# Kernel optimization log

Hardware: AMD Instinct MI355X
Metric: run time of the kernel (lower is better)

Reference implementation:

```python
import jax, jax.numpy as jnp
import numpy as np

LN_EPS = 1e-5

def _proj(x, w, b):
    # 1x1 conv: x [B,C,H,W], w [O,C], b [O]
    return jnp.einsum('bchw,oc->bohw', x, w) + b[None, :, None, None]

def _layernorm(x, w, b):
    # normalize over last dim
    mu = jnp.mean(x, axis=-1, keepdims=True)
    var = jnp.mean(jnp.square(x - mu), axis=-1, keepdims=True)
    return (x - mu) * jax.lax.rsqrt(var + LN_EPS) * w + b

def setup_inputs() -> dict:
    key = jax.random.key(0)
    ks = jax.random.split(key, 12)
    C = 256
    d = {
        's3': jax.random.normal(ks[0], (2, C, 64, 64), jnp.float32),
        's4': jax.random.normal(ks[1], (2, C, 32, 64), jnp.float32),
        's5': jax.random.normal(ks[2], (2, C, 16, 64), jnp.float32),
        'qw': jax.random.normal(ks[3], (C, C), jnp.float32) * 0.02,
        'qb': jax.random.normal(ks[4], (C,), jnp.float32) * 0.02,
        'kw': jax.random.normal(ks[5], (C, C), jnp.float32) * 0.02,
        'kb': jax.random.normal(ks[6], (C,), jnp.float32) * 0.02,
        'vw': jax.random.normal(ks[7], (C, C), jnp.float32) * 0.02,
        'vb': jax.random.normal(ks[8], (C,), jnp.float32) * 0.02,
        'ow': jax.random.normal(ks[9], (C, C), jnp.float32) * 0.02,
        'ob': jax.random.normal(ks[10], (C,), jnp.float32) * 0.02,
        'ln_w': jnp.ones((C,), jnp.float32),
        'ln_b': jnp.zeros((C,), jnp.float32),
    }
    return d

def reference(s3, s4, s5, qw, qb, kw, kb, vw, vb, ow, ob, ln_w, ln_b):
    B, C, H, W = s3.shape
    num_heads = 8
    head_dim = C // num_heads
    scale = head_dim ** -0.5

    q = _proj(s3, qw, qb).reshape(B, C, H * W)            # [B,C,Nq]
    k4 = _proj(s4, kw, kb).reshape(B, C, -1)
    k5 = _proj(s5, kw, kb).reshape(B, C, -1)
    v4 = _proj(s4, vw, vb).reshape(B, C, -1)
    v5 = _proj(s5, vw, vb).reshape(B, C, -1)
    k = jnp.concatenate([k4, k5], axis=-1)                # [B,C,Nk]
    v = jnp.concatenate([v4, v5], axis=-1)

    # [B,C,N] -> [B,h,N,d]
    def split_heads(t):
        Bn, Cn, N = t.shape
        return t.transpose(0, 2, 1).reshape(Bn, N, num_heads, head_dim).transpose(0, 2, 1, 3)

    qh, kh, vh = split_heads(q), split_heads(k), split_heads(v)
    attn = jnp.einsum('bhqd,bhkd->bhqk', qh, kh) * scale
    attn = jax.nn.softmax(attn, axis=-1)
    out = jnp.einsum('bhqk,bhkd->bhqd', attn, vh)         # [B,h,Nq,d]
    out = out.transpose(0, 2, 1, 3).reshape(B, H * W, C)  # [B,Nq,C]
    out = out.transpose(0, 2, 1).reshape(B, C, H, W)
    out = _proj(out, ow, ob)
    out = s3 + out
    out_flat = out.reshape(B, C, H * W).transpose(0, 2, 1)  # [B,N,C]
    out_flat = _layernorm(out_flat, ln_w, ln_b)
    return out_flat.transpose(0, 2, 1).reshape(B, C, H, W)
```

## Files before the change

kernel.cpp:

```cpp
#include <hip/hip_runtime.h>

typedef __bf16 bf16;
typedef __bf16 bf16x4 __attribute__((ext_vector_type(4)));
typedef __bf16 bf16x8 __attribute__((ext_vector_type(8)));
typedef float f32x4 __attribute__((ext_vector_type(4)));
typedef unsigned int u32x4 __attribute__((ext_vector_type(4)));

#define MFMA16 __builtin_amdgcn_mfma_f32_16x16x32_bf16

__device__ __forceinline__ void async16(bf16* lds, const bf16* g) {
    __builtin_amdgcn_global_load_lds((const __attribute__((address_space(1))) unsigned int*)g,
                                     (__attribute__((address_space(3))) unsigned int*)lds, 16, 0, 0);
}

__global__ __launch_bounds__(256) void k_prep(const float* __restrict__ qw, const float* __restrict__ kw,
                                              const float* __restrict__ vw, const float* __restrict__ ow,
                                              bf16* __restrict__ Wb,
                                              const float* __restrict__ s3, const float* __restrict__ s4,
                                              const float* __restrict__ s5,
                                              bf16* __restrict__ s3t, bf16* __restrict__ s45t) {
    __shared__ float T[64][65];
    int bx = blockIdx.x, t = threadIdx.x;
    if (bx < 256) {
        int tt = bx * 256 + t;
        const float* srcs[4] = {qw, kw, vw, ow};
        int which = tt >> 14;
        int idx = (tt & 16383) * 4;
        f32x4 v = *(const f32x4*)(srcs[which] + idx);
        bf16x4 o;
        o[0] = (bf16)v[0]; o[1] = (bf16)v[1]; o[2] = (bf16)v[2]; o[3] = (bf16)v[3];
        *(bf16x4*)(Wb + (size_t)which * 65536 + idx) = o;
        return;
    }
    const float* src; bf16* dst; int N, dstRows, rowOff, x, y, z;
    if (bx < 768)       { int i = bx - 256;  src = s3; dst = s3t;  N = 4096; dstRows = 4096; rowOff = 0;    x = i & 63; y = (i >> 6) & 3; z = i >> 8; }
    else if (bx < 1024) { int i = bx - 768;  src = s4; dst = s45t; N = 2048; dstRows = 3072; rowOff = 0;    x = i & 31; y = (i >> 5) & 3; z = i >> 7; }
    else                { int i = bx - 1024; src = s5; dst = s45t; N = 1024; dstRows = 3072; rowOff = 2048; x = i & 15; y = (i >> 4) & 3; z = i >> 6; }
    int c0 = y * 64, n0 = x * 64, b = z;
    const float* s = src + ((size_t)b * 256 + c0) * N + n0;
#pragma unroll
    for (int i = 0; i < 4; i++) {
        int flat = i * 256 + t;
        int row = flat >> 4;
        int col = (flat & 15) * 4;
        f32x4 v = *(const f32x4*)(s + (size_t)row * N + col);
        T[row][col + 0] = v[0]; T[row][col + 1] = v[1];
        T[row][col + 2] = v[2]; T[row][col + 3] = v[3];
    }
    __syncthreads();
#pragma unroll
    for (int i = 0; i < 4; i++) {
        int flat = i * 256 + t;
        int nrow = flat >> 4;
        int c4 = (flat & 15) * 4;
        bf16x4 o;
        o[0] = (bf16)T[c4 + 0][nrow]; o[1] = (bf16)T[c4 + 1][nrow];
        o[2] = (bf16)T[c4 + 2][nrow]; o[3] = (bf16)T[c4 + 3][nrow];
        *(bf16x4*)(dst + ((size_t)(b * dstRows + rowOff + n0 + nrow)) * 256 + c0 + c4) = o;
    }
}

__global__ __launch_bounds__(256) void k_qkv(const bf16* __restrict__ Wb,
                                             const bf16* __restrict__ s3t, const bf16* __restrict__ s45t,
                                             const float* __restrict__ qb, const float* __restrict__ kb,
                                             const float* __restrict__ vb,
                                             bf16* __restrict__ Qb, bf16* __restrict__ Kb,
                                             bf16* __restrict__ Vtb, float qscale) {
    int i = blockIdx.x;
    int mode, n0, m0, b, Nrows;
    const bf16 *A, *Bt; const float* bias; bf16* Dst; float oscale = 1.0f;
    if (i < 512) {
        mode = 0; A = Wb; Bt = s3t; bias = qb; Dst = Qb; Nrows = 4096; oscale = qscale;
        n0 = (i & 63) * 64; m0 = ((i >> 6) & 3) * 64; b = i >> 8;
    } else if (i < 896) {
        unsigned j = i - 512;
        mode = 0; A = Wb + 65536; Bt = s45t; bias = kb; Dst = Kb; Nrows = 3072;
        n0 = (j % 48u) * 64; unsigned rr = j / 48u; m0 = (rr & 3) * 64; b = rr >> 2;
    } else {
        unsigned j = i - 896;
        mode = 1; A = Wb + 131072; Bt = s45t; bias = vb; Dst = Vtb; Nrows = 3072;
        n0 = (j % 48u) * 64; unsigned rr = j / 48u; m0 = (rr & 3) * 64; b = rr >> 2;
    }
    __shared__ bf16 As[64 * 40];
    __shared__ bf16 Bs[64 * 40];
    int t = threadIdx.x;
    int w = t >> 6, lane = t & 63;
    int lrow = lane & 15, lk = lane >> 4;
    f32x4 acc[4] = {};
    int r = t >> 2, cc = (t & 3) * 8;
    for (int kc = 0; kc < 256; kc += 32) {
        u32x4 va = *(const u32x4*)(A + (size_t)(m0 + r) * 256 + kc + cc);
        u32x4 vbv = *(const u32x4*)(Bt + ((size_t)b * Nrows + n0 + r) * 256 + kc + cc);
        *(u32x4*)(As + r * 40 + cc) = va;
        *(u32x4*)(Bs + r * 40 + cc) = vbv;
        __syncthreads();
        bf16x8 af = *(const bf16x8*)(As + (w * 16 + lrow) * 40 + lk * 8);
#pragma unroll
        for (int ct = 0; ct < 4; ct++) {
            bf16x8 bfr = *(const bf16x8*)(Bs + (ct * 16 + lrow) * 40 + lk * 8);
            acc[ct] = MFMA16(af, bfr, acc[ct], 0, 0, 0);
        }
        __syncthreads();
    }
    int o0 = m0 + w * 16 + lk * 4;
    f32x4 b4 = *(const f32x4*)(bias + o0);
    int head = o0 >> 5, dd = o0 & 31;
#pragma unroll
    for (int ct = 0; ct < 4; ct++) {
        int n = n0 + ct * 16 + lrow;
        if (mode == 0) {
            bf16x4 pv;
#pragma unroll
            for (int j = 0; j < 4; j++) pv[j] = (bf16)((acc[ct][j] + b4[j]) * oscale);
            *(bf16x4*)(Dst + ((size_t)(b * 8 + head) * Nrows + n) * 32 + dd) = pv;
        } else {
            int off = n & 63;
            int np = (n & ~63) + 4 * (off & 15) + (off >> 4);
            size_t base = ((size_t)(b * 8 + head) * 32 + dd) * (size_t)Nrows + np;
#pragma unroll
            for (int j = 0; j < 4; j++) Dst[base + (size_t)j * Nrows] = (bf16)(acc[ct][j] + b4[j]);
        }
    }
}

__global__ __launch_bounds__(256, 6) void k_attn(const bf16* __restrict__ Q, const bf16* __restrict__ K,
                                                 const bf16* __restrict__ Vt,
                                                 float* __restrict__ Opart, float* __restrict__ Lsum) {
    int bh = blockIdx.y;
    int q0 = blockIdx.x * 64;
    int sp = blockIdx.z;
    int kn0 = sp * 1536;
    int t = threadIdx.x, w = t >> 6, lane = t & 63;
    int lrow = lane & 15, lk = lane >> 4;
    __shared__ bf16 Ks[2][64 * 32];
    __shared__ bf16 Vs[2][32 * 64];
    __shared__ bf16 P[4][16 * 72];
    const bf16* kbase = K + (size_t)bh * 3072 * 32;
    const bf16* vbase = Vt + (size_t)bh * 32 * 3072;
    const bf16* kg = kbase + (size_t)(kn0 + w * 16 + (lane >> 2)) * 32 + (lane & 3) * 8;
    int vr = w * 8 + (lane >> 3);
    const bf16* vg = vbase + (size_t)vr * 3072 + kn0 + ((lane & 7) ^ (vr & 7)) * 8;
    bf16* pw = &P[w][0];
    bf16x8 aq = *(const bf16x8*)(Q + ((size_t)bh * 4096 + q0 + w * 16 + lrow) * 32 + lk * 8);
    bf16x8 ones;
#pragma unroll
    for (int j = 0; j < 8; j++) ones[j] = (bf16)1.0f;
    f32x4 accO0 = {}, accO1 = {}, accL = {};
    f32x4 zero = {};
    async16(&Ks[0][w * 512], kg);
    async16(&Vs[0][w * 512], vg);
    __syncthreads();
    for (int c = 0; c < 24; ++c) {
        int buf = c & 1;
        if (c < 23) {
            size_t kc1 = (size_t)(c + 1) * 64;
            async16(&Ks[buf ^ 1][w * 512], kg + kc1 * 32);
            async16(&Vs[buf ^ 1][w * 512], vg + kc1);
        }
        const bf16* ksb = &Ks[buf][0];
        const bf16* vsb = &Vs[buf][0];
        f32x4 s[4];
#pragma unroll
        for (int jt = 0; jt < 4; ++jt) {
            bf16x8 bk = *(const bf16x8*)(ksb + (16 * jt + lrow) * 32 + lk * 8);
            s[jt] = MFMA16(aq, bk, zero, 0, 0, 0);
        }
#pragma unroll
        for (int i = 0; i < 4; ++i) {
            bf16x4 pk;
#pragma unroll
            for (int jt = 0; jt < 4; ++jt) pk[jt] = (bf16)__builtin_amdgcn_exp2f(s[jt][i]);
            *(bf16x4*)(pw + (lk * 4 + i) * 72 + lrow * 4) = pk;
        }
#pragma unroll
        for (int cs = 0; cs < 2; ++cs) {
            bf16x8 ap = *(const bf16x8*)(pw + lrow * 72 + cs * 32 + lk * 8);
            int xb = ((cs * 4 + lk) ^ (lrow & 7)) * 8;
            bf16x8 v0 = *(const bf16x8*)(vsb + lrow * 64 + xb);
            bf16x8 v1 = *(const bf16x8*)(vsb + (16 + lrow) * 64 + xb);
            accO0 = MFMA16(ap, v0, accO0, 0, 0, 0);
            accO1 = MFMA16(ap, v1, accO1, 0, 0, 0);
            accL = MFMA16(ap, ones, accL, 0, 0, 0);
        }
        __syncthreads();
    }
    float* Op = Opart + (size_t)(sp * 16 + bh) * 4096 * 32;
#pragma unroll
    for (int i = 0; i < 4; i++) {
        int q = q0 + w * 16 + lk * 4 + i;
        Op[(size_t)q * 32 + lrow] = accO0[i];
        Op[(size_t)q * 32 + 16 + lrow] = accO1[i];
        if (lrow == 0) Lsum[(size_t)(sp * 16 + bh) * 4096 + q] = accL[i];
    }
}

__global__ __launch_bounds__(256) void k_oproj(const bf16* __restrict__ A, const float* __restrict__ Opart,
                                               const float* __restrict__ Ls, const float* __restrict__ bias,
                                               float* __restrict__ opre) {
    int i = blockIdx.x;
    int n0 = (i & 63) * 64, m0 = ((i >> 6) & 3) * 64, b = i >> 8;
    __shared__ bf16 As[64 * 40];
    __shared__ bf16 Bs[64 * 40];
    int t = threadIdx.x;
    int w = t >> 6, lane = t & 63;
    int lrow = lane & 15, lk = lane >> 4;
    f32x4 acc[4] = {};
    int r = t >> 2, cc = (t & 3) * 8;
    int q = n0 + r;
    for (int kc = 0; kc < 256; kc += 32) {
        int h = kc >> 5, bh = b * 8 + h;
        u32x4 va = *(const u32x4*)(A + (size_t)(m0 + r) * 256 + kc + cc);
        const float* o1 = Opart + ((size_t)bh * 4096 + q) * 32 + cc;
        const float* o2 = Opart + ((size_t)(16 + bh) * 4096 + q) * 32 + cc;
        f32x4 p0 = *(const f32x4*)o1, p1 = *(const f32x4*)(o1 + 4);
        f32x4 r0 = *(const f32x4*)o2, r1 = *(const f32x4*)(o2 + 4);
        float l = Ls[(size_t)bh * 4096 + q] + Ls[(size_t)(16 + bh) * 4096 + q];
        float rl = 1.0f / l;
        bf16x8 bb;
#pragma unroll
        for (int j = 0; j < 4; j++) {
            bb[j] = (bf16)((p0[j] + r0[j]) * rl);
            bb[4 + j] = (bf16)((p1[j] + r1[j]) * rl);
        }
        *(u32x4*)(As + r * 40 + cc) = va;
        *(bf16x8*)(Bs + r * 40 + cc) = bb;
        __syncthreads();
        bf16x8 af = *(const bf16x8*)(As + (w * 16 + lrow) * 40 + lk * 8);
#pragma unroll
        for (int ct = 0; ct < 4; ct++) {
            bf16x8 bfr = *(const bf16x8*)(Bs + (ct * 16 + lrow) * 40 + lk * 8);
            acc[ct] = MFMA16(af, bfr, acc[ct], 0, 0, 0);
        }
        __syncthreads();
    }
    int o0 = m0 + w * 16 + lk * 4;
    f32x4 b4 = *(const f32x4*)(bias + o0);
#pragma unroll
    for (int ct = 0; ct < 4; ct++) {
        int n = n0 + ct * 16 + lrow;
        f32x4 v;
#pragma unroll
        for (int j = 0; j < 4; j++) v[j] = acc[ct][j] + b4[j];
        *(f32x4*)(opre + ((size_t)b * 4096 + n) * 256 + o0) = v;
    }
}

__global__ __launch_bounds__(256) void k_ln(const float* __restrict__ opre, const float* __restrict__ s3,
                                            const float* __restrict__ lnw, const float* __restrict__ lnb,
                                            float* __restrict__ out) {
    int b = blockIdx.y;
    int n0 = blockIdx.x * 32;
    __shared__ float T[32][257];
    __shared__ float mu_s[32], rs_s[32];
    int t = threadIdx.x;
#pragma unroll
    for (int i = 0; i < 8; i++) {
        int flat = i * 256 + t;
        int n = flat >> 6;
        int c = (flat & 63) * 4;
        f32x4 v = *(const f32x4*)(opre + ((size_t)b * 4096 + n0 + n) * 256 + c);
        T[n][c + 0] = v[0]; T[n][c + 1] = v[1]; T[n][c + 2] = v[2]; T[n][c + 3] = v[3];
    }
    __syncthreads();
#pragma unroll
    for (int i = 0; i < 8; i++) {
        int flat = i * 256 + t;
        int c = flat >> 3;
        int n = (flat & 7) * 4;
        f32x4 v = *(const f32x4*)(s3 + ((size_t)b * 256 + c) * 4096 + n0 + n);
        T[n + 0][c] += v[0]; T[n + 1][c] += v[1]; T[n + 2][c] += v[2]; T[n + 3][c] += v[3];
    }
    __syncthreads();
    int w = t >> 6, lane = t & 63;
    for (int j = 0; j < 8; j++) {
        int row = w * 8 + j;
        float x0 = T[row][lane], x1 = T[row][lane + 64];
        float x2 = T[row][lane + 128], x3 = T[row][lane + 192];
        float s = x0 + x1 + x2 + x3;
        float s2 = x0 * x0 + x1 * x1 + x2 * x2 + x3 * x3;
#pragma unroll
        for (int off = 1; off < 64; off <<= 1) {
            s += __shfl_xor(s, off, 64);
            s2 += __shfl_xor(s2, off, 64);
        }
        if (lane == 0) {
            float mu = s * (1.0f / 256.0f);
            float var = s2 * (1.0f / 256.0f) - mu * mu;
            mu_s[row] = mu;
            rs_s[row] = rsqrtf(var + 1e-5f);
        }
    }
    __syncthreads();
    int c = t;
    float wv = lnw[c], bv = lnb[c];
#pragma unroll
    for (int i = 0; i < 8; i++) {
        int n = i * 4;
        f32x4 o;
#pragma unroll
        for (int k = 0; k < 4; k++)
            o[k] = (T[n + k][c] - mu_s[n + k]) * rs_s[n + k] * wv + bv;
        *(f32x4*)(out + ((size_t)b * 256 + c) * 4096 + n0 + n) = o;
    }
}

extern "C" void kernel_launch(void* const* d_in, const int* in_sizes, int n_in,
                              void* d_out, int out_size, void* d_ws, size_t ws_size,
                              hipStream_t stream) {
    const float* s3  = (const float*)d_in[0];
    const float* s4  = (const float*)d_in[1];
    const float* s5  = (const float*)d_in[2];
    const float* qw  = (const float*)d_in[3];
    const float* qb  = (const float*)d_in[4];
    const float* kw  = (const float*)d_in[5];
    const float* kb  = (const float*)d_in[6];
    const float* vw  = (const float*)d_in[7];
    const float* vb  = (const float*)d_in[8];
    const float* ow  = (const float*)d_in[9];
    const float* ob  = (const float*)d_in[10];
    const float* lnw = (const float*)d_in[11];
    const float* lnb = (const float*)d_in[12];
    float* out = (float*)d_out;
    char* ws = (char*)d_ws;

    bf16* Wb    = (bf16*)(ws);
    bf16* s3t   = (bf16*)(ws + (512ull << 10));
    bf16* s45t  = (bf16*)(ws + (4608ull << 10));
    bf16* Qb    = (bf16*)(ws + (7680ull << 10));
    bf16* Kb    = Qb + (2ull * 8 * 4096 * 32);
    bf16* Vtb   = Kb + (2ull * 8 * 3072 * 32);
    float* Opart = (float*)(ws + (17920ull << 10));
    float* Lsum  = (float*)(ws + (34304ull << 10));
    float* opre  = (float*)(ws + (512ull << 10));

    const float qscale = 0.17677669529663688f * 1.4426950408889634f;

    k_prep<<<1152, 256, 0, stream>>>(qw, kw, vw, ow, Wb, s3, s4, s5, s3t, s45t);
    k_qkv<<<1280, 256, 0, stream>>>(Wb, s3t, s45t, qb, kb, vb, Qb, Kb, Vtb, qscale);
    k_attn<<<dim3(64, 16, 2), 256, 0, stream>>>(Qb, Kb, Vtb, Opart, Lsum);
    k_oproj<<<512, 256, 0, stream>>>(Wb + 196608, Opart, Lsum, ob, opre);
    k_ln<<<dim3(128, 2), 256, 0, stream>>>(opre, s3, lnw, lnb, out);
}
```

Before: 167.8 us.

## Keep attention probabilities in registers via transposed QK and fp16 PV MFMA

The attention kernel now computes S transposed (K as the A operand), so the exp'd scores land directly in the register layout needed as the B operand of an fp16 16x16x16 MFMA. This removes the per-wave LDS round trip for P. V is stored as fp16 with an XOR swizzle written by the QKV kernel. Each block now handles 128 queries (two Q fragments per wave) to reuse K/V tiles, with fewer blocks and lower occupancy. Opart is written d-major, and the output projection's loads are changed to match, becoming strided scalar loads.

Measured after the change: 161.9 us. -3.5%, faster.

```diff
diff --git a/kernel.cpp b/kernel.cpp
--- a/kernel.cpp
+++ b/kernel.cpp
@@ -3,12 +3,15 @@
 typedef __bf16 bf16;
 typedef __bf16 bf16x4 __attribute__((ext_vector_type(4)));
 typedef __bf16 bf16x8 __attribute__((ext_vector_type(8)));
+typedef _Float16 f16;
+typedef _Float16 f16x4 __attribute__((ext_vector_type(4)));
 typedef float f32x4 __attribute__((ext_vector_type(4)));
 typedef unsigned int u32x4 __attribute__((ext_vector_type(4)));
 
 #define MFMA16 __builtin_amdgcn_mfma_f32_16x16x32_bf16
-
-__device__ __forceinline__ void async16(bf16* lds, const bf16* g) {
+#define MFMA16F __builtin_amdgcn_mfma_f32_16x16x16f16
+
+__device__ __forceinline__ void async16(void* lds, const void* g) {
     __builtin_amdgcn_global_load_lds((const __attribute__((address_space(1))) unsigned int*)g,
                                      (__attribute__((address_space(3))) unsigned int*)lds, 16, 0, 0);
 }
@@ -65,20 +68,20 @@
                                              const float* __restrict__ qb, const float* __restrict__ kb,
                                              const float* __restrict__ vb,
                                              bf16* __restrict__ Qb, bf16* __restrict__ Kb,
-                                             bf16* __restrict__ Vtb, float qscale) {
+                                             f16* __restrict__ Vtb, float qscale) {
     int i = blockIdx.x;
     int mode, n0, m0, b, Nrows;
-    const bf16 *A, *Bt; const float* bias; bf16* Dst; float oscale = 1.0f;
+    const bf16 *A, *Bt; const float* bias; float oscale = 1.0f;
     if (i < 512) {
-        mode = 0; A = Wb; Bt = s3t; bias = qb; Dst = Qb; Nrows = 4096; oscale = qscale;
+        mode = 0; A = Wb; Bt = s3t; bias = qb; Nrows = 4096; oscale = qscale;
         n0 = (i & 63) * 64; m0 = ((i >> 6) & 3) * 64; b = i >> 8;
     } else if (i < 896) {
         unsigned j = i - 512;
-        mode = 0; A = Wb + 65536; Bt = s45t; bias = kb; Dst = Kb; Nrows = 3072;
+        mode = 0; A = Wb + 65536; Bt = s45t; bias = kb; Nrows = 3072;
         n0 = (j % 48u) * 64; unsigned rr = j / 48u; m0 = (rr & 3) * 64; b = rr >> 2;
     } else {
         unsigned j = i - 896;
-        mode = 1; A = Wb + 131072; Bt = s45t; bias = vb; Dst = Vtb; Nrows = 3072;
+        mode = 1; A = Wb + 131072; Bt = s45t; bias = vb; Nrows = 3072;
         n0 = (j % 48u) * 64; unsigned rr = j / 48u; m0 = (rr & 3) * 64; b = rr >> 2;
     }
     __shared__ bf16 As[64 * 40];
@@ -104,93 +107,105 @@
     }
     int o0 = m0 + w * 16 + lk * 4;
     f32x4 b4 = *(const f32x4*)(bias + o0);
-    int head = o0 >> 5, dd = o0 & 31;
+    int head = o0 >> 5;
 #pragma unroll
     for (int ct = 0; ct < 4; ct++) {
         int n = n0 + ct * 16 + lrow;
         if (mode == 0) {
+            bf16* Dst = (head, Qb);
+            Dst = (oscale == 1.0f && Nrows == 3072) ? Kb : Qb;
+            int dd = o0 & 31;
             bf16x4 pv;
 #pragma unroll
             for (int j = 0; j < 4; j++) pv[j] = (bf16)((acc[ct][j] + b4[j]) * oscale);
             *(bf16x4*)(Dst + ((size_t)(b * 8 + head) * Nrows + n) * 32 + dd) = pv;
         } else {
-            int off = n & 63;
-            int np = (n & ~63) + 4 * (off & 15) + (off >> 4);
-            size_t base = ((size_t)(b * 8 + head) * 32 + dd) * (size_t)Nrows + np;
-#pragma unroll
-            for (int j = 0; j < 4; j++) Dst[base + (size_t)j * Nrows] = (bf16)(acc[ct][j] + b4[j]);
-        }
-    }
-}
-
-__global__ __launch_bounds__(256, 6) void k_attn(const bf16* __restrict__ Q, const bf16* __restrict__ K,
-                                                 const bf16* __restrict__ Vt,
+#pragma unroll
+            for (int j = 0; j < 4; j++) {
+                int dd = (o0 & 31) + j;
+                int kk = ((dd & 7) << 1) | ((dd >> 3) & 1);
+                int u = n & 63, g = u >> 2;
+                int col = n0 + ((g ^ kk) << 2) + (u & 3);
+                Vtb[((size_t)(b * 8 + head) * 32 + dd) * 3072 + col] = (f16)(acc[ct][j] + b4[j]);
+            }
+        }
+    }
+}
+
+__global__ __launch_bounds__(256, 4) void k_attn(const bf16* __restrict__ Q, const bf16* __restrict__ K,
+                                                 const f16* __restrict__ Vt,
                                                  float* __restrict__ Opart, float* __restrict__ Lsum) {
     int bh = blockIdx.y;
-    int q0 = blockIdx.x * 64;
+    int q0 = blockIdx.x * 128;
     int sp = blockIdx.z;
     int kn0 = sp * 1536;
     int t = threadIdx.x, w = t >> 6, lane = t & 63;
     int lrow = lane & 15, lk = lane >> 4;
     __shared__ bf16 Ks[2][64 * 32];
-    __shared__ bf16 Vs[2][32 * 64];
-    __shared__ bf16 P[4][16 * 72];
+    __shared__ f16 Vs[2][32 * 64];
     const bf16* kbase = K + (size_t)bh * 3072 * 32;
-    const bf16* vbase = Vt + (size_t)bh * 32 * 3072;
+    const f16* vbase = Vt + (size_t)bh * 32 * 3072;
     const bf16* kg = kbase + (size_t)(kn0 + w * 16 + (lane >> 2)) * 32 + (lane & 3) * 8;
-    int vr = w * 8 + (lane >> 3);
-    const bf16* vg = vbase + (size_t)vr * 3072 + kn0 + ((lane & 7) ^ (vr & 7)) * 8;
-    bf16* pw = &P[w][0];
-    bf16x8 aq = *(const bf16x8*)(Q + ((size_t)bh * 4096 + q0 + w * 16 + lrow) * 32 + lk * 8);
-    bf16x8 ones;
-#pragma unroll
-    for (int j = 0; j < 8; j++) ones[j] = (bf16)1.0f;
-    f32x4 accO0 = {}, accO1 = {}, accL = {};
+    const f16* vg = vbase + (size_t)(w * 8 + (lane >> 3)) * 3072 + kn0 + (lane & 7) * 8;
+    const bf16* qrow = Q + ((size_t)bh * 4096 + q0 + w * 32 + lrow) * 32 + lk * 8;
+    bf16x8 aq0 = *(const bf16x8*)(qrow);
+    bf16x8 aq1 = *(const bf16x8*)(qrow + 16 * 32);
+    f16x4 ones;
+    ones[0] = (f16)1.f; ones[1] = (f16)1.f; ones[2] = (f16)1.f; ones[3] = (f16)1.f;
+    f32x4 accO[2][2] = {};
+    f32x4 accL[2] = {};
     f32x4 zero = {};
+    int kk2 = ((lrow & 7) << 1) | (lrow >> 3);
     async16(&Ks[0][w * 512], kg);
     async16(&Vs[0][w * 512], vg);
     __syncthreads();
     for (int c = 0; c < 24; ++c) {
         int buf = c & 1;
         if (c < 23) {
-            size_t kc1 = (size_t)(c + 1) * 64;
-            async16(&Ks[buf ^ 1][w * 512], kg + kc1 * 32);
+            int kc1 = (c + 1) * 64;
+            async16(&Ks[buf ^ 1][w * 512], kg + (size_t)kc1 * 32);
             async16(&Vs[buf ^ 1][w * 512], vg + kc1);
         }
         const bf16* ksb = &Ks[buf][0];
-        const bf16* vsb = &Vs[buf][0];
-        f32x4 s[4];
+        const f16* vsb = &Vs[buf][0];
+        f32x4 s0[4], s1[4];
 #pragma unroll
         for (int jt = 0; jt < 4; ++jt) {
-            bf16x8 bk = *(const bf16x8*)(ksb + (16 * jt + lrow) * 32 + lk * 8);
-            s[jt] = MFMA16(aq, bk, zero, 0, 0, 0);
-        }
-#pragma unroll
-        for (int i = 0; i < 4; ++i) {
-            bf16x4 pk;
-#pragma unroll
-            for (int jt = 0; jt < 4; ++jt) pk[jt] = (bf16)__builtin_amdgcn_exp2f(s[jt][i]);
-            *(bf16x4*)(pw + (lk * 4 + i) * 72 + lrow * 4) = pk;
-        }
-#pragma unroll
-        for (int cs = 0; cs < 2; ++cs) {
-            bf16x8 ap = *(const bf16x8*)(pw + lrow * 72 + cs * 32 + lk * 8);
-            int xb = ((cs * 4 + lk) ^ (lrow & 7)) * 8;
-            bf16x8 v0 = *(const bf16x8*)(vsb + lrow * 64 + xb);
-            bf16x8 v1 = *(const bf16x8*)(vsb + (16 + lrow) * 64 + xb);
-            accO0 = MFMA16(ap, v0, accO0, 0, 0, 0);
-            accO1 = MFMA16(ap, v1, accO1, 0, 0, 0);
-            accL = MFMA16(ap, ones, accL, 0, 0, 0);
-        }
-        __syncthreads();
-    }
-    float* Op = Opart + (size_t)(sp * 16 + bh) * 4096 * 32;
-#pragma unroll
-    for (int i = 0; i < 4; i++) {
-        int q = q0 + w * 16 + lk * 4 + i;
-        Op[(size_t)q * 32 + lrow] = accO0[i];
-        Op[(size_t)q * 32 + 16 + lrow] = accO1[i];
-        if (lrow == 0) Lsum[(size_t)(sp * 16 + bh) * 4096 + q] = accL[i];
+            bf16x8 kf = *(const bf16x8*)(ksb + (16 * jt + lrow) * 32 + lk * 8);
+            s0[jt] = MFMA16(kf, aq0, zero, 0, 0, 0);
+            s1[jt] = MFMA16(kf, aq1, zero, 0, 0, 0);
+        }
+#pragma unroll
+        for (int jt = 0; jt < 4; ++jt) {
+            f16x4 p0, p1;
+#pragma unroll
+            for (int i = 0; i < 4; ++i) {
+                p0[i] = (f16)__builtin_amdgcn_exp2f(s0[jt][i]);
+                p1[i] = (f16)__builtin_amdgcn_exp2f(s1[jt][i]);
+            }
+            int gcol = (((jt << 2) | lk) ^ kk2) << 2;
+            f16x4 vf0 = *(const f16x4*)(vsb + lrow * 64 + gcol);
+            f16x4 vf1 = *(const f16x4*)(vsb + (16 + lrow) * 64 + gcol);
+            accO[0][0] = MFMA16F(vf0, p0, accO[0][0], 0, 0, 0);
+            accO[0][1] = MFMA16F(vf1, p0, accO[0][1], 0, 0, 0);
+            accO[1][0] = MFMA16F(vf0, p1, accO[1][0], 0, 0, 0);
+            accO[1][1] = MFMA16F(vf1, p1, accO[1][1], 0, 0, 0);
+            accL[0] = MFMA16F(ones, p0, accL[0], 0, 0, 0);
+            accL[1] = MFMA16F(ones, p1, accL[1], 0, 0, 0);
+        }
+        __syncthreads();
+    }
+    int sb = sp * 16 + bh;
+    float* Ob = Opart + (size_t)sb * 32 * 4096;
+#pragma unroll
+    for (int qg = 0; qg < 2; ++qg) {
+        int q = q0 + w * 32 + qg * 16 + lrow;
+#pragma unroll
+        for (int dh = 0; dh < 2; ++dh)
+#pragma unroll
+            for (int i = 0; i < 4; ++i)
+                Ob[(size_t)(dh * 16 + lk * 4 + i) * 4096 + q] = accO[qg][dh][i];
+        if (lane < 16) Lsum[(size_t)sb * 4096 + q] = accL[qg][0];
     }
 }
 
@@ -210,18 +225,14 @@
     for (int kc = 0; kc < 256; kc += 32) {
         int h = kc >> 5, bh = b * 8 + h;
         u32x4 va = *(const u32x4*)(A + (size_t)(m0 + r) * 256 + kc + cc);
-        const float* o1 = Opart + ((size_t)bh * 4096 + q) * 32 + cc;
-        const float* o2 = Opart + ((size_t)(16 + bh) * 4096 + q) * 32 + cc;
-        f32x4 p0 = *(const f32x4*)o1, p1 = *(const f32x4*)(o1 + 4);
-        f32x4 r0 = *(const f32x4*)o2, r1 = *(const f32x4*)(o2 + 4);
+        const float* o1 = Opart + ((size_t)bh * 32 + cc) * 4096 + q;
+        const float* o2 = o1 + (size_t)16 * 32 * 4096;
         float l = Ls[(size_t)bh * 4096 + q] + Ls[(size_t)(16 + bh) * 4096 + q];
         float rl = 1.0f / l;
         bf16x8 bb;
 #pragma unroll
-        for (int j = 0; j < 4; j++) {
-            bb[j] = (bf16)((p0[j] + r0[j]) * rl);
-            bb[4 + j] = (bf16)((p1[j] + r1[j]) * rl);
-        }
+        for (int u = 0; u < 8; ++u)
+            bb[u] = (bf16)((o1[(size_t)u * 4096] + o2[(size_t)u * 4096]) * rl);
         *(u32x4*)(As + r * 40 + cc) = va;
         *(bf16x8*)(Bs + r * 40 + cc) = bb;
         __syncthreads();
@@ -328,7 +339,7 @@
     bf16* s45t  = (bf16*)(ws + (4608ull << 10));
     bf16* Qb    = (bf16*)(ws + (7680ull << 10));
     bf16* Kb    = Qb + (2ull * 8 * 4096 * 32);
-    bf16* Vtb   = Kb + (2ull * 8 * 3072 * 32);
+    f16*  Vtb   = (f16*)(Kb + (2ull * 8 * 3072 * 32));
     float* Opart = (float*)(ws + (17920ull << 10));
     float* Lsum  = (float*)(ws + (34304ull << 10));
     float* opre  = (float*)(ws + (512ull << 10));
@@ -337,7 +348,7 @@
 
     k_prep<<<1152, 256, 0, stream>>>(qw, kw, vw, ow, Wb, s3, s4, s5, s3t, s45t);
     k_qkv<<<1280, 256, 0, stream>>>(Wb, s3t, s45t, qb, kb, vb, Qb, Kb, Vtb, qscale);
-    k_attn<<<dim3(64, 16, 2), 256, 0, stream>>>(Qb, Kb, Vtb, Opart, Lsum);
+    k_attn<<<dim3(32, 16, 2), 256, 0, stream>>>(Qb, Kb, Vtb, Opart, Lsum);
     k_oproj<<<512, 256, 0, stream>>>(Wb + 196608, Opart, Lsum, ob, opre);
     k_ln<<<dim3(128, 2), 256, 0, stream>>>(opre, s3, lnw, lnb, out);
 }
```
